# Performance work log

Hardware: AMD Instinct MI355X
Metric: run time of the kernel (lower is better)

## Reference

```python
import jax, jax.numpy as jnp
import numpy as np

BLOCK = 64
EPS = 1e-6
N_HEADS = 16


def _rope(t, cos, sin):
    # t: (B,S,H,hd); cos/sin: (S, hd//2) -> broadcast (1,S,1,hd//2)
    B, S, H, hd = t.shape
    tr = t.reshape(B, S, H, hd // 2, 2)
    t0, t1 = tr[..., 0], tr[..., 1]
    c = cos[None, :, None, :]
    s = sin[None, :, None, :]
    o0 = t0 * c - t1 * s
    o1 = t0 * s + t1 * c
    return jnp.stack([o0, o1], axis=-1).reshape(B, S, H, hd)


def setup_inputs() -> dict:
    key = jax.random.key(0)
    ks = jax.random.split(key, 6)
    B, S, D = 1, 2048, 2048
    hd = D // N_HEADS
    x = jax.random.normal(ks[0], (B, S, D), dtype=jnp.float32)
    # rotary table: theta_i = 10000^(-2i/hd)
    inv_freq = 1.0 / (10000.0 ** (jnp.arange(0, hd, 2, dtype=jnp.float32) / hd))
    t = jnp.arange(S, dtype=jnp.float32)
    freqs = jnp.outer(t, inv_freq)  # (S, hd//2)
    freqs_cos = jnp.cos(freqs)
    freqs_sin = jnp.sin(freqs)
    std = 0.02
    Wq = jax.random.normal(ks[1], (D, D), dtype=jnp.float32) * std
    Wk = jax.random.normal(ks[2], (D, D), dtype=jnp.float32) * std
    Wv = jax.random.normal(ks[3], (D, D), dtype=jnp.float32) * std
    Wo = jax.random.normal(ks[4], (D, D), dtype=jnp.float32) * std
    mask = jnp.ones((1, 1), dtype=bool)  # non-None mask => no masking in original code
    return {"x": x, "freqs_cos": freqs_cos, "freqs_sin": freqs_sin,
            "Wq": Wq, "Wk": Wk, "Wv": Wv, "Wo": Wo, "mask": mask}


def reference(x, freqs_cos, freqs_sin, Wq, Wk, Wv, Wo, mask):
    B, S, D = x.shape
    H = N_HEADS
    hd = D // H
    scale = hd ** -0.5
    nb = S // BLOCK

    q = (x @ Wq.T).reshape(B, S, H, hd)
    k = (x @ Wk.T).reshape(B, S, H, hd)
    v = (x @ Wv.T).reshape(B, S, H, hd)
    q = _rope(q, freqs_cos, freqs_sin)
    k = _rope(k, freqs_cos, freqs_sin)

    # block views: (B, nb, BLOCK, H, hd)
    qb = q.reshape(B, nb, BLOCK, H, hd)
    kb = k.reshape(B, nb, BLOCK, H, hd)
    vb = v.reshape(B, nb, BLOCK, H, hd)

    # per-(i,j) block scores: (B, nb_i, nb_j, H, BLOCK_q, BLOCK_k)
    s = jnp.einsum('binhd,bjmhd->bijhnm', qb, kb) * scale
    # NOTE: original module (mask is not None path) applies NO causal mask and
    # uses the per-block local max (no running-max rescale) -- reproduced exactly.
    m = jnp.max(s, axis=-1, keepdims=True)
    p = jnp.exp(s - m)
    # denominator: sum of per-block row sums over all j blocks -> (B, nb, H, BLOCK)
    L = p.sum(axis=-1).sum(axis=2)
    # numerator: sum over j blocks of p @ v -> (B, nb, BLOCK, H, hd)
    O = jnp.einsum('bijhnm,bjmhd->binhd', p, vb).reshape(B, S, H, hd)
    Lr = L.transpose(0, 1, 3, 2).reshape(B, S, H, 1)  # (B,S,H,1)
    O = O / (Lr + EPS)
    return O.reshape(B, S, D) @ Wo.T
```

## Files before the change

### kernel.cpp

```cpp
#include <hip/hip_runtime.h>
#include <hip/hip_bf16.h>
#include <math.h>

#define SEQ 2048
#define DM  2048
#define NH  16
#define HD  128
#define SCALE 0.08838834764831845f

typedef __bf16 bf16_t;
typedef __bf16 bf16x8 __attribute__((ext_vector_type(8)));
typedef __bf16 bf16x4 __attribute__((ext_vector_type(4)));
typedef float  f32x4  __attribute__((ext_vector_type(4)));
typedef int    i32x4  __attribute__((ext_vector_type(4)));

typedef const __attribute__((address_space(1))) void* gas_ptr;
typedef __attribute__((address_space(3))) void* las_ptr;

__device__ __forceinline__ void gload_lds16(const void* g, void* l) {
    __builtin_amdgcn_global_load_lds((gas_ptr)g, (las_ptr)l, 16, 0, 0);
}

__device__ __forceinline__ f32x4 mfma_bf16(bf16x8 a, bf16x8 b, f32x4 c) {
    return __builtin_amdgcn_mfma_f32_16x16x32_bf16(a, b, c, 0, 0, 0);
}

__device__ __forceinline__ unsigned cvtpk_bf16(float lo, float hi) {
    unsigned d;
    asm("v_cvt_pk_bf16_f32 %0, %1, %2" : "=v"(d) : "v"(lo), "v"(hi));
    return d;
}

__device__ __forceinline__ bf16x8 read_frag64(const bf16_t* lds, int row, int k) {
    int chunk = (k >> 3) ^ (row & 7);
    return *(const bf16x8*)(lds + row * 64 + chunk * 8);
}
__device__ __forceinline__ bf16x8 read_frag128(const bf16_t* lds, int row, int k) {
    int chunk = k >> 3;
    chunk = (chunk & 8) | ((chunk ^ row) & 7);
    return *(const bf16x8*)(lds + row * 128 + chunk * 8);
}
__device__ __forceinline__ bf16x8 read_slab(const bf16_t* sl, int row, int g) {
    int j = g ^ ((row >> 1) & 3);
    return *(const bf16x8*)(sl + row * 32 + j * 8);
}

__global__ __launch_bounds__(256) void cvt5(
    const float* __restrict__ s0, const float* __restrict__ s1,
    const float* __restrict__ s2, const float* __restrict__ s3,
    const float* __restrict__ s4,
    bf16_t* __restrict__ d0, bf16_t* __restrict__ d1, bf16_t* __restrict__ d2,
    bf16_t* __restrict__ d3, bf16_t* __restrict__ d4)
{
    int which = blockIdx.y;
    const float* s; bf16_t* d;
    switch (which) {
        case 0: s = s0; d = d0; break;
        case 1: s = s1; d = d1; break;
        case 2: s = s2; d = d2; break;
        case 3: s = s3; d = d3; break;
        default: s = s4; d = d4; break;
    }
    size_t idx = ((size_t)blockIdx.x * 256 + threadIdx.x) * 4;
    float4 v = *(const float4*)(s + idx);
    bf16x4 o = { (bf16_t)v.x, (bf16_t)v.y, (bf16_t)v.z, (bf16_t)v.w };
    *(bf16x4*)(d + idx) = o;
}

#define BARX() asm volatile("s_barrier" ::: "memory")
#define VMW8 asm volatile("s_waitcnt vmcnt(8)" ::: "memory")
#define VMW4 asm volatile("s_waitcnt vmcnt(4)" ::: "memory")
#define VMW0 asm volatile("s_waitcnt vmcnt(0)" ::: "memory")
#define NOGATE

__global__ __launch_bounds__(512, 2) void qkv_pipe(
    const bf16_t* __restrict__ A,
    const bf16_t* __restrict__ B0, const bf16_t* __restrict__ B1,
    const bf16_t* __restrict__ B2,
    bf16_t* __restrict__ Oq, bf16_t* __restrict__ Ok, bf16_t* __restrict__ Ov,
    const float* __restrict__ fcos, const float* __restrict__ fsin)
{
    __shared__ bf16_t lds[65536];

    const int tid = threadIdx.x;
    const int lane = tid & 63;
    const int w = tid >> 6;
    const int wm = w >> 2;
    const int wn = w & 3;
    const int g4 = lane >> 4, r15 = lane & 15;

    const int bm = blockIdx.x;
    const int bny = blockIdx.y;
    const int sel = bny >> 3;
    const int bnl = bny & 7;
    const bf16_t* Bp = (sel == 0) ? B0 : (sel == 1) ? B1 : B2;

    const size_t arow0 = (size_t)bm * 256;
    const size_t brow0 = (size_t)bnl * 256;

    const int row0 = tid >> 2;
    const int kj0  = (tid & 3) ^ ((row0 >> 1) & 3);
    const bf16_t* pA = A  + (arow0 + row0) * DM + kj0 * 8;
    const bf16_t* pB = Bp + (brow0 + row0) * DM + kj0 * 8;
    char* ldsb = (char*)lds;
    const int off0 = tid * 16;
    const int off1 = 8192 + tid * 16;

    #define STAGE_HT(S) do { if ((S) < 128) {                                   \
        const int T_ = (S) >> 2, a_ = (S) & 3;                                  \
        const int ko_ = T_ * 64 + ((a_ >> 1) << 5);                             \
        char* dst_ = ldsb + (((T_ & 1) << 16) | ((a_ & 1) << 15) | ((a_ >> 1) << 14)); \
        const bf16_t* s0_ = (a_ & 1) ? pB : pA;                                 \
        gload_lds16(s0_ + ko_, dst_ + off0);                                    \
        gload_lds16(s0_ + 128 * DM + ko_, dst_ + off1);                         \
    } } while (0)

    const bf16_t* b0A0 = lds;
    const bf16_t* b0A1 = lds + 8192;
    const bf16_t* b0B0 = lds + 16384;
    const bf16_t* b0B1 = lds + 24576;
    const bf16_t* b1A0 = lds + 32768;
    const bf16_t* b1A1 = lds + 40960;
    const bf16_t* b1B0 = lds + 49152;
    const bf16_t* b1B1 = lds + 57344;

    f32x4 acc[8][4] = {};

    #define PHASE(ASL, BSL, MH, SIDX, GATE, READB)                              \
    {                                                                           \
        _Pragma("unroll")                                                       \
        for (int m = 0; m < 4; ++m)                                             \
            af[m] = read_slab((ASL), wm * 128 + (MH) * 64 + m * 16 + r15, g4);  \
        if (READB) {                                                            \
            _Pragma("unroll")                                                   \
            for (int n = 0; n < 4; ++n)                                         \
                bfr[n] = read_slab((BSL), wn * 64 + n * 16 + r15, g4);          \
        }                                                                       \
        STAGE_HT(SIDX);                                                         \
        GATE;                                                                   \
        BARX();                                                                 \
        __builtin_amdgcn_s_setprio(1);                                          \
        _Pragma("unroll")                                                       \
        for (int m = 0; m < 4; ++m)                                             \
            _Pragma("unroll")                                                   \
            for (int n = 0; n < 4; ++n)                                         \
                acc[(MH) * 4 + m][n] = mfma_bf16(af[m], bfr[n], acc[(MH) * 4 + m][n]); \
        __builtin_amdgcn_s_setprio(0);                                          \
        BARX();                                                                 \
    }

    STAGE_HT(0); STAGE_HT(1); STAGE_HT(2); STAGE_HT(3); STAGE_HT(4); STAGE_HT(5);
    VMW8;
    BARX();

    for (int i = 0; i < 15; ++i) {
        const int s0 = 6 + i * 8;
        bf16x8 af[4], bfr[4];
        PHASE(b0A0, b0B0, 0, s0 + 0, NOGATE, 1)
        PHASE(b0A0, b0B0, 1, s0 + 1, VMW8,   0)
        PHASE(b0A1, b0B1, 0, s0 + 2, NOGATE, 1)
        PHASE(b0A1, b0B1, 1, s0 + 3, VMW8,   0)
        PHASE(b1A0, b1B0, 0, s0 + 4, NOGATE, 1)
        PHASE(b1A0, b1B0, 1, s0 + 5, VMW8,   0)
        PHASE(b1A1, b1B1, 0, s0 + 6, NOGATE, 1)
        PHASE(b1A1, b1B1, 1, s0 + 7, VMW8,   0)
    }
    {
        const int s0 = 6 + 15 * 8;
        bf16x8 af[4], bfr[4];
        PHASE(b0A0, b0B0, 0, s0 + 0, NOGATE, 1)
        PHASE(b0A0, b0B0, 1, s0 + 1, VMW8,   0)
        PHASE(b0A1, b0B1, 0, s0 + 2, NOGATE, 1)
        PHASE(b0A1, b0B1, 1, s0 + 3, VMW4,   0)
        PHASE(b1A0, b1B0, 0, s0 + 4, NOGATE, 1)
        PHASE(b1A0, b1B0, 1, s0 + 5, VMW0,   0)
        PHASE(b1A1, b1B1, 0, s0 + 6, NOGATE, 1)
        PHASE(b1A1, b1B1, 1, s0 + 7, NOGATE, 0)
    }
    #undef PHASE
    #undef STAGE_HT

    const int r0 = bm * 256 + wm * 128;
    const int c0 = bnl * 256 + wn * 64;

    if (sel == 2) {
        #pragma unroll
        for (int m = 0; m < 8; ++m) {
            int rowb = r0 + m * 16 + g4 * 4;
            #pragma unroll
            for (int n = 0; n < 4; ++n) {
                int col = c0 + n * 16 + r15;
                bf16x4 pk = { (bf16_t)acc[m][n][0], (bf16_t)acc[m][n][1],
                              (bf16_t)acc[m][n][2], (bf16_t)acc[m][n][3] };
                *(bf16x4*)&Ov[(size_t)col * SEQ + rowb] = pk;
            }
        }
    } else {
        bf16_t* dst = (sel == 0) ? Oq : Ok;
        #pragma unroll
        for (int m = 0; m < 8; ++m) {
            int rowb = r0 + m * 16 + g4 * 4;
            #pragma unroll
            for (int n = 0; n < 4; ++n) {
                int col = c0 + n * 16 + r15;
                int f = (col & (HD - 1)) >> 1;
                float sgn = (col & 1) ? 1.0f : -1.0f;
                #pragma unroll
                for (int r = 0; r < 4; ++r) {
                    float mine = acc[m][n][r];
                    float other = __shfl_xor(mine, 1);
                    float cc = fcos[(rowb + r) * (HD / 2) + f];
                    float ss = fsin[(rowb + r) * (HD / 2) + f];
                    float o = mine * cc + sgn * other * ss;
                    dst[(size_t)(rowb + r) * DM + col] = (bf16_t)o;
                }
            }
        }
    }
}

__global__ __launch_bounds__(256) void gemm_fin(
    const bf16_t* __restrict__ A, const bf16_t* __restrict__ B0,
    float* __restrict__ Of)
{
    __shared__ bf16_t lA[128 * 64];
    __shared__ bf16_t lB[128 * 64];

    const int tid = threadIdx.x;
    const int lane = tid & 63;
    const int w = tid >> 6;
    const int wm = w >> 1, wn = w & 1;
    const int g = lane >> 4, r15 = lane & 15;

    const int bm = blockIdx.x;
    const int bn = blockIdx.y;

    f32x4 acc[4][4] = {};

    const size_t arow0 = (size_t)bm * 128;
    const size_t brow0 = (size_t)bn * 128;

    for (int kt = 0; kt < DM / 64; ++kt) {
        const int k0 = kt * 64;
        #pragma unroll
        for (int i = 0; i < 4; ++i) {
            int c = i * 256 + tid;
            int row = c >> 3;
            int ck = (c ^ row) & 7;
            const bf16_t* ga = A + (arow0 + row) * DM + k0 + ck * 8;
            gload_lds16(ga, (char*)lA + (i * 256 + w * 64) * 16);
            const bf16_t* gb = B0 + (brow0 + row) * DM + k0 + ck * 8;
            gload_lds16(gb, (char*)lB + (i * 256 + w * 64) * 16);
        }
        __syncthreads();
        #pragma unroll
        for (int kk = 0; kk < 2; ++kk) {
            bf16x8 af[4], bfr[4];
            #pragma unroll
            for (int m = 0; m < 4; ++m)
                af[m] = read_frag64(lA, wm * 64 + m * 16 + r15, kk * 32 + g * 8);
            #pragma unroll
            for (int n = 0; n < 4; ++n)
                bfr[n] = read_frag64(lB, wn * 64 + n * 16 + r15, kk * 32 + g * 8);
            #pragma unroll
            for (int m = 0; m < 4; ++m)
                #pragma unroll
                for (int n = 0; n < 4; ++n)
                    acc[m][n] = mfma_bf16(af[m], bfr[n], acc[m][n]);
        }
        __syncthreads();
    }

    const int r0 = bm * 128 + wm * 64;
    const int c0 = bn * 128 + wn * 64;
    #pragma unroll
    for (int m = 0; m < 4; ++m) {
        int rowb = r0 + m * 16 + g * 4;
        #pragma unroll
        for (int n = 0; n < 4; ++n) {
            int col = c0 + n * 16 + r15;
            #pragma unroll
            for (int r = 0; r < 4; ++r)
                Of[(size_t)(rowb + r) * DM + col] = acc[m][n][r];
        }
    }
}

__global__ __launch_bounds__(256, 2) void attn_k2(
    const bf16_t* __restrict__ Q, const bf16_t* __restrict__ Kb,
    const bf16_t* __restrict__ Vt, bf16_t* __restrict__ Ob)
{
    __shared__ bf16_t lk[2 * 64 * 128];
    __shared__ bf16_t lv[2 * 128 * 64];

    const int tid = threadIdx.x;
    const int lane = tid & 63;
    const int w = tid >> 6;
    const int g = lane >> 4, r15 = lane & 15;
    const int qb = blockIdx.x, h = blockIdx.y;

    const int lo = g & 1, hb = g >> 1;
    const int e_src = (lo << 5) + r15;
    const int o_src = e_src + 16;
    const int sA = hb ? o_src : e_src;
    const int sB = hb ? e_src : o_src;

    bf16x8 qf[4];
    {
        const bf16_t* qrow = Q + (size_t)(qb * 64 + w * 16 + r15) * DM + h * HD + g * 8;
        #pragma unroll
        for (int ks = 0; ks < 4; ++ks)
            qf[ks] = *(const bf16x8*)(qrow + ks * 32);
    }

    f32x4 oacc[8] = {};
    float Lsum = 0.f;

    #define STAGE_KV(JJ, BUF)                                                     \
    {                                                                             \
        _Pragma("unroll")                                                         \
        for (int i = 0; i < 4; ++i) {                                             \
            int c = i * 256 + tid;                                                \
            int row = c >> 4, ckl = c & 15;                                       \
            int ck = (ckl & 8) | ((ckl ^ row) & 7);                               \
            const bf16_t* gk = Kb + (size_t)((JJ) * 64 + row) * DM + h * HD + ck * 8; \
            gload_lds16(gk, (char*)lk + (BUF) * 16384 + (i * 256 + w * 64) * 16); \
        }                                                                         \
        _Pragma("unroll")                                                         \
        for (int i = 0; i < 4; ++i) {                                             \
            int c = i * 256 + tid;                                                \
            int row = c >> 3;                                                     \
            int ck = (c ^ row) & 7;                                               \
            const bf16_t* gv = Vt + (size_t)(h * HD + row) * SEQ + (JJ) * 64 + ck * 8; \
            gload_lds16(gv, (char*)lv + (BUF) * 16384 + (i * 256 + w * 64) * 16); \
        }                                                                         \
    }

    STAGE_KV(0, 0);
    asm volatile("s_waitcnt vmcnt(0)" ::: "memory");
    __builtin_amdgcn_s_barrier();

    for (int j = 0; j < SEQ / 64; ++j) {
        const int cur = j & 1;
        const bf16_t* lkc = lk + cur * 8192;
        const bf16_t* lvc = lv + cur * 8192;
        if (j < SEQ / 64 - 1) STAGE_KV(j + 1, cur ^ 1);

        f32x4 sacc[4] = {};
        __builtin_amdgcn_s_setprio(1);
        #pragma unroll
        for (int ks = 0; ks < 4; ++ks) {
            #pragma unroll
            for (int n = 0; n < 4; ++n) {
                bf16x8 kf = read_frag128(lkc, n * 16 + r15, ks * 32 + g * 8);
                sacc[n] = mfma_bf16(kf, qf[ks], sacc[n]);
            }
        }
        __builtin_amdgcn_s_setprio(0);

        float mx0 = fmaxf(fmaxf(sacc[0][0], sacc[0][1]), fmaxf(sacc[0][2], sacc[0][3]));
        float mx1 = fmaxf(fmaxf(sacc[1][0], sacc[1][1]), fmaxf(sacc[1][2], sacc[1][3]));
        float mx2 = fmaxf(fmaxf(sacc[2][0], sacc[2][1]), fmaxf(sacc[2][2], sacc[2][3]));
        float mx3 = fmaxf(fmaxf(sacc[3][0], sacc[3][1]), fmaxf(sacc[3][2], sacc[3][3]));
        float mx = fmaxf(fmaxf(mx0, mx1), fmaxf(mx2, mx3));
        mx = fmaxf(mx, __shfl_xor(mx, 16));
        mx = fmaxf(mx, __shfl_xor(mx, 32));

        float p[4][4];
        float ls = 0.f;
        #pragma unroll
        for (int n = 0; n < 4; ++n)
            #pragma unroll
            for (int r = 0; r < 4; ++r) {
                float pv = __expf((sacc[n][r] - mx) * SCALE);
                p[n][r] = pv;
                ls += pv;
            }
        Lsum += ls;

        unsigned D00 = cvtpk_bf16(p[0][0], p[0][1]), D01 = cvtpk_bf16(p[0][2], p[0][3]);
        unsigned D10 = cvtpk_bf16(p[1][0], p[1][1]), D11 = cvtpk_bf16(p[1][2], p[1][3]);
        unsigned D20 = cvtpk_bf16(p[2][0], p[2][1]), D21 = cvtpk_bf16(p[2][2], p[2][3]);
        unsigned D30 = cvtpk_bf16(p[3][0], p[3][1]), D31 = cvtpk_bf16(p[3][2], p[3][3]);

        unsigned r0 = __shfl((int)(lo ? D10 : D00), sA);
        unsigned r1 = __shfl((int)(lo ? D11 : D01), sA);
        unsigned r2 = __shfl((int)(lo ? D00 : D10), sB);
        unsigned r3 = __shfl((int)(lo ? D01 : D11), sB);
        unsigned r4 = __shfl((int)(lo ? D30 : D20), sA);
        unsigned r5 = __shfl((int)(lo ? D31 : D21), sA);
        unsigned r6 = __shfl((int)(lo ? D20 : D30), sB);
        unsigned r7 = __shfl((int)(lo ? D21 : D31), sB);
        i32x4 w0, w1;
        w0[0] = (int)(hb ? r2 : r0);  w0[1] = (int)(hb ? r3 : r1);
        w0[2] = (int)(hb ? r0 : r2);  w0[3] = (int)(hb ? r1 : r3);
        w1[0] = (int)(hb ? r6 : r4);  w1[1] = (int)(hb ? r7 : r5);
        w1[2] = (int)(hb ? r4 : r6);  w1[3] = (int)(hb ? r5 : r7);
        bf16x8 pa0 = __builtin_bit_cast(bf16x8, w0);
        bf16x8 pa1 = __builtin_bit_cast(bf16x8, w1);

        __builtin_amdgcn_s_setprio(1);
        #pragma unroll
        for (int n = 0; n < 8; ++n) {
            bf16x8 bv = read_frag64(lvc, n * 16 + r15, g * 8);
            oacc[n] = mfma_bf16(pa0, bv, oacc[n]);
        }
        #pragma unroll
        for (int n = 0; n < 8; ++n) {
            bf16x8 bv = read_frag64(lvc, n * 16 + r15, 32 + g * 8);
            oacc[n] = mfma_bf16(pa1, bv, oacc[n]);
        }
        __builtin_amdgcn_s_setprio(0);

        asm volatile("s_waitcnt vmcnt(0)" ::: "memory");
        __builtin_amdgcn_s_barrier();
    }

    float L = Lsum;
    L += __shfl_xor(L, 16);
    L += __shfl_xor(L, 32);
    float inv = 1.0f / (L + 1e-6f);
    float invr[4];
    #pragma unroll
    for (int r = 0; r < 4; ++r)
        invr[r] = __shfl(inv, g * 4 + r);

    #pragma unroll
    for (int n = 0; n < 8; ++n) {
        int col = h * HD + n * 16 + r15;
        int rowb = qb * 64 + w * 16 + g * 4;
        #pragma unroll
        for (int r = 0; r < 4; ++r)
            Ob[(size_t)(rowb + r) * DM + col] = (bf16_t)(oacc[n][r] * invr[r]);
    }
}

extern "C" void kernel_launch(void* const* d_in, const int* in_sizes, int n_in,
                              void* d_out, int out_size, void* d_ws, size_t ws_size,
                              hipStream_t stream)
{
    const float* x    = (const float*)d_in[0];
    const float* fcos = (const float*)d_in[1];
    const float* fsin = (const float*)d_in[2];
    const float* Wq   = (const float*)d_in[3];
    const float* Wk   = (const float*)d_in[4];
    const float* Wv   = (const float*)d_in[5];
    const float* Wo   = (const float*)d_in[6];
    float* out = (float*)d_out;

    const size_t NE = (size_t)DM * SEQ;
    bf16_t* ws  = (bf16_t*)d_ws;
    bf16_t* xb  = ws;
    bf16_t* wqb = ws + 1 * NE;
    bf16_t* wkb = ws + 2 * NE;
    bf16_t* wvb = ws + 3 * NE;
    bf16_t* wob = ws + 4 * NE;
    bf16_t* qr  = ws + 5 * NE;
    bf16_t* kr  = ws + 6 * NE;
    bf16_t* vt  = ws + 7 * NE;
    bf16_t* ob  = ws + 8 * NE;

    hipLaunchKernelGGL(cvt5, dim3(4096, 5), dim3(256), 0, stream,
                       x, Wq, Wk, Wv, Wo, xb, wqb, wkb, wvb, wob);

    hipLaunchKernelGGL(qkv_pipe, dim3(8, 24), dim3(512), 0, stream,
                       xb, wqb, wkb, wvb, qr, kr, vt, fcos, fsin);

    hipLaunchKernelGGL(attn_k2, dim3(32, 16), dim3(256), 0, stream,
                       qr, kr, vt, ob);

    hipLaunchKernelGGL(gemm_fin, dim3(16, 16), dim3(256), 0, stream,
                       ob, wob, out);
}
```

Before: 179.7 us.

## Retile attention to two query tiles per wave, shrink output GEMM tile, swap QKV grid order

The attention kernel now runs 2 waves per block, each handling 32 query rows (two 16-row tiles), so each K/V fragment read from LDS feeds two MFMAs. This is meant to cut LDS traffic per MFMA, at the cost of more registers and fewer waves. The output projection GEMM tile drops from 128x128 to 128x64, doubling the block count for better CU coverage. The QKV grid is transposed so consecutive blocks share the same A row tile, which changes L2 reuse.

```diff
diff --git a/kernel.cpp b/kernel.cpp
--- a/kernel.cpp
+++ b/kernel.cpp
@@ -89,8 +89,8 @@
     const int wn = w & 3;
     const int g4 = lane >> 4, r15 = lane & 15;
 
-    const int bm = blockIdx.x;
-    const int bny = blockIdx.y;
+    const int bm = blockIdx.y;
+    const int bny = blockIdx.x;
     const int sel = bny >> 3;
     const int bnl = bny & 7;
     const bf16_t* Bp = (sel == 0) ? B0 : (sel == 1) ? B1 : B2;
@@ -224,7 +224,7 @@
     float* __restrict__ Of)
 {
     __shared__ bf16_t lA[128 * 64];
-    __shared__ bf16_t lB[128 * 64];
+    __shared__ bf16_t lB[64 * 64];
 
     const int tid = threadIdx.x;
     const int lane = tid & 63;
@@ -235,10 +235,10 @@
     const int bm = blockIdx.x;
     const int bn = blockIdx.y;
 
-    f32x4 acc[4][4] = {};
+    f32x4 acc[4][2] = {};
 
     const size_t arow0 = (size_t)bm * 128;
-    const size_t brow0 = (size_t)bn * 128;
+    const size_t brow0 = (size_t)bn * 64;
 
     for (int kt = 0; kt < DM / 64; ++kt) {
         const int k0 = kt * 64;
@@ -249,35 +249,41 @@
             int ck = (c ^ row) & 7;
             const bf16_t* ga = A + (arow0 + row) * DM + k0 + ck * 8;
             gload_lds16(ga, (char*)lA + (i * 256 + w * 64) * 16);
+        }
+        #pragma unroll
+        for (int i = 0; i < 2; ++i) {
+            int c = i * 256 + tid;
+            int row = c >> 3;
+            int ck = (c ^ row) & 7;
             const bf16_t* gb = B0 + (brow0 + row) * DM + k0 + ck * 8;
             gload_lds16(gb, (char*)lB + (i * 256 + w * 64) * 16);
         }
         __syncthreads();
         #pragma unroll
         for (int kk = 0; kk < 2; ++kk) {
-            bf16x8 af[4], bfr[4];
+            bf16x8 af[4], bfr[2];
             #pragma unroll
             for (int m = 0; m < 4; ++m)
                 af[m] = read_frag64(lA, wm * 64 + m * 16 + r15, kk * 32 + g * 8);
             #pragma unroll
-            for (int n = 0; n < 4; ++n)
-                bfr[n] = read_frag64(lB, wn * 64 + n * 16 + r15, kk * 32 + g * 8);
+            for (int n = 0; n < 2; ++n)
+                bfr[n] = read_frag64(lB, wn * 32 + n * 16 + r15, kk * 32 + g * 8);
             #pragma unroll
             for (int m = 0; m < 4; ++m)
                 #pragma unroll
-                for (int n = 0; n < 4; ++n)
+                for (int n = 0; n < 2; ++n)
                     acc[m][n] = mfma_bf16(af[m], bfr[n], acc[m][n]);
         }
         __syncthreads();
     }
 
     const int r0 = bm * 128 + wm * 64;
-    const int c0 = bn * 128 + wn * 64;
+    const int c0 = bn * 64 + wn * 32;
     #pragma unroll
     for (int m = 0; m < 4; ++m) {
         int rowb = r0 + m * 16 + g * 4;
         #pragma unroll
-        for (int n = 0; n < 4; ++n) {
+        for (int n = 0; n < 2; ++n) {
             int col = c0 + n * 16 + r15;
             #pragma unroll
             for (int r = 0; r < 4; ++r)
@@ -286,7 +292,7 @@
     }
 }
 
-__global__ __launch_bounds__(256, 2) void attn_k2(
+__global__ __launch_bounds__(128, 1) void attn_k4(
     const bf16_t* __restrict__ Q, const bf16_t* __restrict__ Kb,
     const bf16_t* __restrict__ Vt, bf16_t* __restrict__ Ob)
 {
@@ -305,34 +311,35 @@
     const int sA = hb ? o_src : e_src;
     const int sB = hb ? e_src : o_src;
 
-    bf16x8 qf[4];
-    {
-        const bf16_t* qrow = Q + (size_t)(qb * 64 + w * 16 + r15) * DM + h * HD + g * 8;
+    bf16x8 qf[2][4];
+    #pragma unroll
+    for (int u = 0; u < 2; ++u) {
+        const bf16_t* qrow = Q + (size_t)(qb * 64 + w * 32 + u * 16 + r15) * DM + h * HD + g * 8;
         #pragma unroll
         for (int ks = 0; ks < 4; ++ks)
-            qf[ks] = *(const bf16x8*)(qrow + ks * 32);
-    }
-
-    f32x4 oacc[8] = {};
-    float Lsum = 0.f;
+            qf[u][ks] = *(const bf16x8*)(qrow + ks * 32);
+    }
+
+    f32x4 oacc[2][8] = {};
+    float Lsum[2] = {0.f, 0.f};
 
     #define STAGE_KV(JJ, BUF)                                                     \
     {                                                                             \
         _Pragma("unroll")                                                         \
-        for (int i = 0; i < 4; ++i) {                                             \
-            int c = i * 256 + tid;                                                \
+        for (int i = 0; i < 8; ++i) {                                             \
+            int c = i * 128 + tid;                                                \
             int row = c >> 4, ckl = c & 15;                                       \
             int ck = (ckl & 8) | ((ckl ^ row) & 7);                               \
             const bf16_t* gk = Kb + (size_t)((JJ) * 64 + row) * DM + h * HD + ck * 8; \
-            gload_lds16(gk, (char*)lk + (BUF) * 16384 + (i * 256 + w * 64) * 16); \
+            gload_lds16(gk, (char*)lk + (BUF) * 16384 + (i * 128 + w * 64) * 16); \
         }                                                                         \
         _Pragma("unroll")                                                         \
-        for (int i = 0; i < 4; ++i) {                                             \
-            int c = i * 256 + tid;                                                \
+        for (int i = 0; i < 8; ++i) {                                             \
+            int c = i * 128 + tid;                                                \
             int row = c >> 3;                                                     \
             int ck = (c ^ row) & 7;                                               \
             const bf16_t* gv = Vt + (size_t)(h * HD + row) * SEQ + (JJ) * 64 + ck * 8; \
-            gload_lds16(gv, (char*)lv + (BUF) * 16384 + (i * 256 + w * 64) * 16); \
+            gload_lds16(gv, (char*)lv + (BUF) * 16384 + (i * 128 + w * 64) * 16); \
         }                                                                         \
     }
 
@@ -346,69 +353,73 @@
         const bf16_t* lvc = lv + cur * 8192;
         if (j < SEQ / 64 - 1) STAGE_KV(j + 1, cur ^ 1);
 
-        f32x4 sacc[4] = {};
+        f32x4 sacc[2][4] = {};
         __builtin_amdgcn_s_setprio(1);
         #pragma unroll
         for (int ks = 0; ks < 4; ++ks) {
             #pragma unroll
             for (int n = 0; n < 4; ++n) {
                 bf16x8 kf = read_frag128(lkc, n * 16 + r15, ks * 32 + g * 8);
-                sacc[n] = mfma_bf16(kf, qf[ks], sacc[n]);
+                sacc[0][n] = mfma_bf16(kf, qf[0][ks], sacc[0][n]);
+                sacc[1][n] = mfma_bf16(kf, qf[1][ks], sacc[1][n]);
             }
         }
         __builtin_amdgcn_s_setprio(0);
 
-        float mx0 = fmaxf(fmaxf(sacc[0][0], sacc[0][1]), fmaxf(sacc[0][2], sacc[0][3]));
-        float mx1 = fmaxf(fmaxf(sacc[1][0], sacc[1][1]), fmaxf(sacc[1][2], sacc[1][3]));
-        float mx2 = fmaxf(fmaxf(sacc[2][0], sacc[2][1]), fmaxf(sacc[2][2], sacc[2][3]));
-        float mx3 = fmaxf(fmaxf(sacc[3][0], sacc[3][1]), fmaxf(sacc[3][2], sacc[3][3]));
-        float mx = fmaxf(fmaxf(mx0, mx1), fmaxf(mx2, mx3));
-        mx = fmaxf(mx, __shfl_xor(mx, 16));
-        mx = fmaxf(mx, __shfl_xor(mx, 32));
-
-        float p[4][4];
-        float ls = 0.f;
-        #pragma unroll
-        for (int n = 0; n < 4; ++n)
-            #pragma unroll
-            for (int r = 0; r < 4; ++r) {
-                float pv = __expf((sacc[n][r] - mx) * SCALE);
-                p[n][r] = pv;
-                ls += pv;
-            }
-        Lsum += ls;
-
-        unsigned D00 = cvtpk_bf16(p[0][0], p[0][1]), D01 = cvtpk_bf16(p[0][2], p[0][3]);
-        unsigned D10 = cvtpk_bf16(p[1][0], p[1][1]), D11 = cvtpk_bf16(p[1][2], p[1][3]);
-        unsigned D20 = cvtpk_bf16(p[2][0], p[2][1]), D21 = cvtpk_bf16(p[2][2], p[2][3]);
-        unsigned D30 = cvtpk_bf16(p[3][0], p[3][1]), D31 = cvtpk_bf16(p[3][2], p[3][3]);
-
-        unsigned r0 = __shfl((int)(lo ? D10 : D00), sA);
-        unsigned r1 = __shfl((int)(lo ? D11 : D01), sA);
-        unsigned r2 = __shfl((int)(lo ? D00 : D10), sB);
-        unsigned r3 = __shfl((int)(lo ? D01 : D11), sB);
-        unsigned r4 = __shfl((int)(lo ? D30 : D20), sA);
-        unsigned r5 = __shfl((int)(lo ? D31 : D21), sA);
-        unsigned r6 = __shfl((int)(lo ? D20 : D30), sB);
-        unsigned r7 = __shfl((int)(lo ? D21 : D31), sB);
-        i32x4 w0, w1;
-        w0[0] = (int)(hb ? r2 : r0);  w0[1] = (int)(hb ? r3 : r1);
-        w0[2] = (int)(hb ? r0 : r2);  w0[3] = (int)(hb ? r1 : r3);
-        w1[0] = (int)(hb ? r6 : r4);  w1[1] = (int)(hb ? r7 : r5);
-        w1[2] = (int)(hb ? r4 : r6);  w1[3] = (int)(hb ? r5 : r7);
-        bf16x8 pa0 = __builtin_bit_cast(bf16x8, w0);
-        bf16x8 pa1 = __builtin_bit_cast(bf16x8, w1);
+        bf16x8 pa0[2], pa1[2];
+        #pragma unroll
+        for (int u = 0; u < 2; ++u) {
+            float mx0 = fmaxf(fmaxf(sacc[u][0][0], sacc[u][0][1]), fmaxf(sacc[u][0][2], sacc[u][0][3]));
+            float mx1 = fmaxf(fmaxf(sacc[u][1][0], sacc[u][1][1]), fmaxf(sacc[u][1][2], sacc[u][1][3]));
+            float mx2 = fmaxf(fmaxf(sacc[u][2][0], sacc[u][2][1]), fmaxf(sacc[u][2][2], sacc[u][2][3]));
+            float mx3 = fmaxf(fmaxf(sacc[u][3][0], sacc[u][3][1]), fmaxf(sacc[u][3][2], sacc[u][3][3]));
+            float mx = fmaxf(fmaxf(mx0, mx1), fmaxf(mx2, mx3));
+            mx = fmaxf(mx, __shfl_xor(mx, 16));
+            mx = fmaxf(mx, __shfl_xor(mx, 32));
+
+            float p[4][4];
+            float ls = 0.f;
+            #pragma unroll
+            for (int n = 0; n < 4; ++n)
+                #pragma unroll
+                for (int r = 0; r < 4; ++r) {
+                    float pv = __expf((sacc[u][n][r] - mx) * SCALE);
+                    p[n][r] = pv;
+                    ls += pv;
+                }
+            Lsum[u] += ls;
+
+            unsigned D00 = cvtpk_bf16(p[0][0], p[0][1]), D01 = cvtpk_bf16(p[0][2], p[0][3]);
+            unsigned D10 = cvtpk_bf16(p[1][0], p[1][1]), D11 = cvtpk_bf16(p[1][2], p[1][3]);
+            unsigned D20 = cvtpk_bf16(p[2][0], p[2][1]), D21 = cvtpk_bf16(p[2][2], p[2][3]);
+            unsigned D30 = cvtpk_bf16(p[3][0], p[3][1]), D31 = cvtpk_bf16(p[3][2], p[3][3]);
+
+            unsigned r0 = __shfl((int)(lo ? D10 : D00), sA);
+            unsigned r1 = __shfl((int)(lo ? D11 : D01), sA);
+            unsigned r2 = __shfl((int)(lo ? D00 : D10), sB);
+            unsigned r3 = __shfl((int)(lo ? D01 : D11), sB);
+            unsigned r4 = __shfl((int)(lo ? D30 : D20), sA);
+            unsigned r5 = __shfl((int)(lo ? D31 : D21), sA);
+            unsigned r6 = __shfl((int)(lo ? D20 : D30), sB);
+            unsigned r7 = __shfl((int)(lo ? D21 : D31), sB);
+            i32x4 w0, w1;
+            w0[0] = (int)(hb ? r2 : r0);  w0[1] = (int)(hb ? r3 : r1);
+            w0[2] = (int)(hb ? r0 : r2);  w0[3] = (int)(hb ? r1 : r3);
+            w1[0] = (int)(hb ? r6 : r4);  w1[1] = (int)(hb ? r7 : r5);
+            w1[2] = (int)(hb ? r4 : r6);  w1[3] = (int)(hb ? r5 : r7);
+            pa0[u] = __builtin_bit_cast(bf16x8, w0);
+            pa1[u] = __builtin_bit_cast(bf16x8, w1);
+        }
 
         __builtin_amdgcn_s_setprio(1);
         #pragma unroll
         for (int n = 0; n < 8; ++n) {
-            bf16x8 bv = read_frag64(lvc, n * 16 + r15, g * 8);
-            oacc[n] = mfma_bf16(pa0, bv, oacc[n]);
-        }
-        #pragma unroll
-        for (int n = 0; n < 8; ++n) {
-            bf16x8 bv = read_frag64(lvc, n * 16 + r15, 32 + g * 8);
-            oacc[n] = mfma_bf16(pa1, bv, oacc[n]);
+            bf16x8 bv0 = read_frag64(lvc, n * 16 + r15, g * 8);
+            oacc[0][n] = mfma_bf16(pa0[0], bv0, oacc[0][n]);
+            oacc[1][n] = mfma_bf16(pa0[1], bv0, oacc[1][n]);
+            bf16x8 bv1 = read_frag64(lvc, n * 16 + r15, 32 + g * 8);
+            oacc[0][n] = mfma_bf16(pa1[0], bv1, oacc[0][n]);
+            oacc[1][n] = mfma_bf16(pa1[1], bv1, oacc[1][n]);
         }
         __builtin_amdgcn_s_setprio(0);
 
@@ -416,22 +427,25 @@
         __builtin_amdgcn_s_barrier();
     }
 
-    float L = Lsum;
-    L += __shfl_xor(L, 16);
-    L += __shfl_xor(L, 32);
-    float inv = 1.0f / (L + 1e-6f);
-    float invr[4];
     #pragma unroll
-    for (int r = 0; r < 4; ++r)
-        invr[r] = __shfl(inv, g * 4 + r);
-
-    #pragma unroll
-    for (int n = 0; n < 8; ++n) {
-        int col = h * HD + n * 16 + r15;
-        int rowb = qb * 64 + w * 16 + g * 4;
+    for (int u = 0; u < 2; ++u) {
+        float L = Lsum[u];
+        L += __shfl_xor(L, 16);
+        L += __shfl_xor(L, 32);
+        float inv = 1.0f / (L + 1e-6f);
+        float invr[4];
         #pragma unroll
         for (int r = 0; r < 4; ++r)
-            Ob[(size_t)(rowb + r) * DM + col] = (bf16_t)(oacc[n][r] * invr[r]);
+            invr[r] = __shfl(inv, g * 4 + r);
+
+        #pragma unroll
+        for (int n = 0; n < 8; ++n) {
+            int col = h * HD + n * 16 + r15;
+            int rowb = qb * 64 + w * 32 + u * 16 + g * 4;
+            #pragma unroll
+            for (int r = 0; r < 4; ++r)
+                Ob[(size_t)(rowb + r) * DM + col] = (bf16_t)(oacc[u][n][r] * invr[r]);
+        }
     }
 }
 
@@ -463,12 +477,12 @@
     hipLaunchKernelGGL(cvt5, dim3(4096, 5), dim3(256), 0, stream,
                        x, Wq, Wk, Wv, Wo, xb, wqb, wkb, wvb, wob);
 
-    hipLaunchKernelGGL(qkv_pipe, dim3(8, 24), dim3(512), 0, stream,
+    hipLaunchKernelGGL(qkv_pipe, dim3(24, 8), dim3(512), 0, stream,
                        xb, wqb, wkb, wvb, qr, kr, vt, fcos, fsin);
 
-    hipLaunchKernelGGL(attn_k2, dim3(32, 16), dim3(256), 0, stream,
+    hipLaunchKernelGGL(attn_k4, dim3(32, 16), dim3(128), 0, stream,
                        qr, kr, vt, ob);
 
-    hipLaunchKernelGGL(gemm_fin, dim3(16, 16), dim3(256), 0, stream,
+    hipLaunchKernelGGL(gemm_fin, dim3(16, 32), dim3(256), 0, stream,
                        ob, wob, out);
 }
```

Result: slower. 189.1 us (+5.2%).
